# Kernel optimization log

Measured on AMD Instinct MI355X. Metric: run time of the kernel, lower is better.

## Reference

```python
import jax, jax.numpy as jnp
import numpy as np

V, D, B, P = 50000, 128, 1024, 50
N, E = B * P, B * P
SCALE = 12.0


def _norm(x):
    return jnp.linalg.norm(x, axis=-1, keepdims=True)


def setup_inputs():
    key = jax.random.key(0)
    ks = jax.random.split(key, 32)
    stdv = 1.0 / np.sqrt(D)

    def u(k, shape):
        return jax.random.uniform(k, shape, minval=-stdv, maxval=stdv, dtype=jnp.float32)

    iid = jax.random.randint(ks[0], (N,), 0, V)
    # edges stay inside each session's node block [g*P, (g+1)*P)
    base = jnp.repeat(jnp.arange(B) * P, P)
    edge_src = base + jax.random.randint(ks[1], (E,), 0, P)
    edge_dst = base + jax.random.randint(ks[2], (E,), 0, P)
    node_gid = jnp.repeat(jnp.arange(B), P)          # session id per node
    last_nodes = jnp.arange(B) * P + (P - 1)          # nodes with data['last']==1
    edge_w = jax.random.uniform(ks[3], (E,), minval=0.1, maxval=1.0)
    edge_t = jax.random.uniform(ks[4], (E,))
    params = dict(
        embedding=u(ks[5], (V, D)),
        W1=u(ks[6], (D, 2 * D)), W2=u(ks[7], (D, 2 * D)),
        gru_wih=u(ks[8], (3 * D, 4 * D)), gru_whh=u(ks[9], (3 * D, D)),
        gru_bih=u(ks[10], (3 * D,)), gru_bhh=u(ks[11], (3 * D,)),
        Wxr=u(ks[12], (D, D)), bxr=u(ks[13], (D,)),
        Wxz=u(ks[14], (D, D)), bxz=u(ks[15], (D,)),
        Wxh=u(ks[16], (D, D)), bxh=u(ks[17], (D,)),
        Whr=u(ks[18], (D, D)), bhr=u(ks[19], (D,)),
        Whz=u(ks[20], (D, D)), bhz=u(ks[21], (D,)),
        Whh=u(ks[22], (D, D)), bhh=u(ks[23], (D,)),
        fc_u=u(ks[24], (D, D)),
        fc_vw=u(ks[25], (D, D)), fc_vb=u(ks[26], (D,)),
        fc_e=u(ks[27], (D,)),
        fc_sr=u(ks[28], (2 * D, D)),
    )
    return dict(iid=iid, edge_src=edge_src, edge_dst=edge_dst, node_gid=node_gid,
                last_nodes=last_nodes, edge_w=edge_w, edge_t=edge_t, **params)


def reference(iid, edge_src, edge_dst, node_gid, last_nodes, edge_w, edge_t,
              embedding, W1, W2, gru_wih, gru_whh, gru_bih, gru_bhh,
              Wxr, bxr, Wxz, bxz, Wxh, bxh, Whr, bhr, Whz, bhz, Whh, bhh,
              fc_u, fc_vw, fc_vb, fc_e, fc_sr):
    segN = lambda d, ids: jax.ops.segment_sum(d, ids, num_segments=N)
    feat = embedding[iid]
    feat = feat / (_norm(feat) + 1e-12)

    # --- GGNNLayer (num_layers=1): weighted-mean over in-edges and reversed graph ---
    ws_in = segN(edge_w, edge_dst)
    ws_out = segN(edge_w, edge_src)
    m_in = segN(feat[edge_src] * edge_w[:, None], edge_dst)
    m_out = segN(feat[edge_dst] * edge_w[:, None], edge_src)
    neigh1 = m_in / jnp.where(ws_in > 0, ws_in, 1.0)[:, None]   # zero-degree -> 0 (DGL default)
    neigh2 = m_out / jnp.where(ws_out > 0, ws_out, 1.0)[:, None]
    hn = jnp.concatenate([neigh1 @ W1, neigh2 @ W2], axis=1)    # [N, 4D]
    gi = hn @ gru_wih.T + gru_bih
    gh = feat @ gru_whh.T + gru_bhh
    ir, iz, inn = jnp.split(gi, 3, axis=1)
    hr, hz, hnn = jnp.split(gh, 3, axis=1)
    r = jax.nn.sigmoid(ir + hr)
    z = jax.nn.sigmoid(iz + hz)
    n = jnp.tanh(inn + r * hnn)
    feat = (1.0 - z) * n + z * feat                              # GRUCell update
    feat = feat / jnp.maximum(_norm(feat), 1e-12)                # F.normalize

    # --- GraphGRUODE: one RK4 step on [0, t_end]; per-eval time-filtered symmetric GCN ---
    x = feat
    no_self = edge_src != edge_dst

    def gcn(h, em, W, b):
        # DGL GraphConv norm='both' on the masked graph + its reverse edges
        deg = segN(em, edge_src) + segN(em, edge_dst)
        nrm = jnp.maximum(deg, 1.0) ** -0.5
        hs = h * nrm[:, None]
        me = em[:, None]
        agg = segN(hs[edge_src] * me, edge_dst) + segN(hs[edge_dst] * me, edge_src)
        return (agg * nrm[:, None]) @ W + b

    def f(tv, h):
        em = ((edge_t <= tv) & no_self).astype(h.dtype)
        xr = gcn(x, em, Wxr, bxr)
        xz = gcn(x, em, Wxz, bxz)
        xh = gcn(x, em, Wxh, bxh)
        r_ = jax.nn.sigmoid(xr + gcn(h, em, Whr, bhr))
        z_ = jax.nn.sigmoid(xz + gcn(h, em, Whz, bhz))
        u_ = jnp.tanh(xh + gcn(r_ * h, em, Whh, bhh))
        dh = (1.0 - z_) * (u_ - h)
        return dh / jnp.maximum(_norm(dh), 1e-12)                # F.normalize

    dt = edge_t.max()
    k1 = f(jnp.float32(0.0), feat)
    k2 = f(dt * 0.5, feat + dt * 0.5 * k1)
    k3 = f(dt * 0.5, feat + dt * 0.5 * k2)
    k4 = f(dt, feat + dt * k3)
    feat = feat + (dt / 6.0) * (k1 + 2.0 * k2 + 2.0 * k3 + k4)
    feat = feat / _norm(feat)                                    # torch code divides with no eps here

    # --- AttnReadout (batch_norm disabled, fc_out is None) ---
    fu = feat @ fc_u
    fv = feat[last_nodes] @ fc_vw + fc_vb                        # [B, D]
    e = jax.nn.sigmoid(fu + fv[node_gid]) @ fc_e                 # [N]
    emax = jax.ops.segment_max(e, node_gid, num_segments=B)
    ee = jnp.exp(e - emax[node_gid])
    alpha = ee / jax.ops.segment_sum(ee, node_gid, num_segments=B)[node_gid]
    sr_g = jax.ops.segment_sum(feat * alpha[:, None], node_gid, num_segments=B)
    sr = jnp.concatenate([feat[last_nodes], sr_g], axis=1) @ fc_sr
    sr = sr / (_norm(sr) + 1e-12)

    target = embedding / (_norm(embedding) + 1e-12)
    logits = sr @ target.T                                       # [B, V]
    return jax.nn.log_softmax(SCALE * logits, axis=-1)
```

## Files before the change

kernel.cpp:

```cpp
#include <hip/hip_runtime.h>
#include <math.h>

constexpr int V_ = 50000, D_ = 128, B_ = 1024, P_ = 50;
constexpr int N_ = 51200, E_ = 51200;
constexpr long long NS_ = (long long)N_ * D_;
constexpr float SCALE_ = 12.0f;
constexpr int NBN_L = (V_ + 127) / 128;
constexpr int NBN_P = 392;

typedef unsigned short u16;
typedef __attribute__((ext_vector_type(8))) unsigned short u16x8;
typedef __attribute__((ext_vector_type(8))) __bf16 bf16x8;
typedef __attribute__((ext_vector_type(4))) float f32x4;

static __device__ __forceinline__ float wsum(float v) {
    #pragma unroll
    for (int o = 32; o; o >>= 1) v += __shfl_xor(v, o, 64);
    return v;
}
static __device__ __forceinline__ float wmax(float v) {
    #pragma unroll
    for (int o = 32; o; o >>= 1) v = fmaxf(v, __shfl_xor(v, o, 64));
    return v;
}
static __device__ __forceinline__ float fsig(float x) { return 1.f / (1.f + __expf(-x)); }
static __device__ __forceinline__ float ftanh(float x) { return 2.f / (1.f + __expf(-2.f * x)) - 1.f; }
static __device__ __forceinline__ u16 f2b(float x) {
    unsigned u = __float_as_uint(x);
    u += 0x7fffu + ((u >> 16) & 1u);
    return (u16)(u >> 16);
}
static __device__ __forceinline__ float b2f(u16 u) {
    return __uint_as_float(((unsigned)u) << 16);
}
static __device__ __forceinline__ float redlr(float v) {
    v += __shfl_xor(v, 1, 64); v += __shfl_xor(v, 2, 64);
    v += __shfl_xor(v, 4, 64); v += __shfl_xor(v, 8, 64);
    return v;
}

__global__ void k_embcv(const float* __restrict__ emb, u16* __restrict__ embb,
                        float* __restrict__ rnv) {
    int row = blockIdx.x * 4 + (threadIdx.x >> 6);
    if (row >= V_) return;
    int l = threadIdx.x & 63;
    const float* p = emb + (long long)row * D_;
    float a = p[l], b = p[l + 64];
    float ss = wsum(a * a + b * b);
    if (l == 0) rnv[row] = 1.f / (sqrtf(ss) + 1e-12f);
    u16* q = embb + (long long)row * D_;
    q[l] = f2b(a); q[l + 64] = f2b(b);
}

__global__ void k_dtmax(const float* __restrict__ et, float* __restrict__ dt) {
    __shared__ float s[1024];
    float m = 0.f;
    for (int i = threadIdx.x; i < E_; i += 1024) m = fmaxf(m, et[i]);
    s[threadIdx.x] = m; __syncthreads();
    for (int o = 512; o; o >>= 1) {
        if (threadIdx.x < o) s[threadIdx.x] = fmaxf(s[threadIdx.x], s[threadIdx.x + o]);
        __syncthreads();
    }
    if (threadIdx.x == 0) *dt = s[0];
}

__global__ void k_csr(const int* __restrict__ esrc, const int* __restrict__ edst,
                      const float* __restrict__ et, const float* __restrict__ dtp,
                      float* __restrict__ csr_nrm, int* __restrict__ csr_soff,
                      int* __restrict__ csr_snbr) {
    __shared__ int ses[P_], sed[P_], sdeg[P_], soff[P_ + 1];
    int mg = blockIdx.x, t = threadIdx.x;
    int mask = mg >> 10;
    int g = mg & 1023;
    int n0 = g * P_;
    float tfac = (mask == 0) ? 0.f : ((mask == 1) ? 0.5f : 1.f);
    float tv = tfac * dtp[0];
    if (t < P_) {
        int E0 = g * P_ + t;
        int s = esrc[E0] - n0, d = edst[E0] - n0;
        bool ml = (s != d) && (et[E0] <= tv);
        ses[t] = ml ? s : -1;
        sed[t] = ml ? d : -1;
    }
    __syncthreads();
    if (t < P_) {
        int dg = 0;
        for (int e = 0; e < P_; e++) dg += (ses[e] == t) + (sed[e] == t);
        sdeg[t] = dg;
        csr_nrm[(long long)mg * P_ + t] = rsqrtf(fmaxf((float)dg, 1.f));
    }
    __syncthreads();
    {
        int v = (t < P_) ? sdeg[t] : 0;
        int inc = v;
        #pragma unroll
        for (int o = 1; o < 64; o <<= 1) {
            int u = __shfl_up(inc, o, 64);
            if (t >= o) inc += u;
        }
        if (t < P_) soff[t] = inc - v;
        if (t == P_ - 1) soff[P_] = inc;
    }
    __syncthreads();
    if (t <= P_) csr_soff[(long long)mg * 64 + t] = soff[t];
    if (t < P_) {
        int c = soff[t];
        for (int e = 0; e < P_; e++) {
            if (ses[e] == t) csr_snbr[(long long)mg * 100 + (c++)] = sed[e];
            if (sed[e] == t) csr_snbr[(long long)mg * 100 + (c++)] = ses[e];
        }
    }
}

__global__ void k_feat0(const u16* __restrict__ embb, const float* __restrict__ rnv,
                        const int* __restrict__ iid, u16* __restrict__ featb) {
    int row = blockIdx.x * 4 + (threadIdx.x >> 6);
    int l = threadIdx.x & 63;
    int id = iid[row];
    const u16* p = embb + (long long)id * D_;
    float s = rnv[id];
    u16* qb = featb + (long long)row * D_;
    qb[l] = f2b(b2f(p[l]) * s); qb[l + 64] = f2b(b2f(p[l + 64]) * s);
}

__global__ void k_aggA_g(const int* __restrict__ esrc, const int* __restrict__ edst,
                         const float* __restrict__ ew, const u16* __restrict__ featb,
                         u16* __restrict__ m_in, u16* __restrict__ m_out) {
    __shared__ float sfeat[P_ * D_];
    __shared__ float smin[P_ * D_];
    __shared__ float smout[P_ * D_];
    __shared__ int ses[P_], sed[P_];
    __shared__ float sw[P_], swin[P_], swout[P_];
    int g = blockIdx.x, t = threadIdx.x;
    int n0 = g * P_;
    long long base = (long long)n0 * D_;
    for (int i = t; i < P_ * D_; i += 256) {
        sfeat[i] = b2f(featb[base + i]);
        smin[i] = 0.f; smout[i] = 0.f;
    }
    if (t < P_) {
        int E0 = g * P_ + t;
        ses[t] = esrc[E0] - n0;
        sed[t] = edst[E0] - n0;
        sw[t] = ew[E0];
    }
    __syncthreads();
    int d = t & 127;
    for (int e = 0; e < P_; e++) {
        int ls = ses[e], ld = sed[e];
        float w = sw[e];
        if (t < 128) smin[ld * D_ + d] += sfeat[ls * D_ + d] * w;
        else         smout[ls * D_ + d] += sfeat[ld * D_ + d] * w;
    }
    if (t < P_) {
        float wi = 0.f, wo = 0.f;
        for (int e = 0; e < P_; e++) {
            if (sed[e] == t) wi += sw[e];
            if (ses[e] == t) wo += sw[e];
        }
        swin[t] = (wi > 0.f) ? 1.f / wi : 1.f;
        swout[t] = (wo > 0.f) ? 1.f / wo : 1.f;
    }
    __syncthreads();
    for (int i = t; i < P_ * D_; i += 256) {
        int n = i >> 7;
        m_in[base + i] = f2b(smin[i] * swin[n]);
        m_out[base + i] = f2b(smout[i] * swout[n]);
    }
}

__global__ void k_prec_all(const float* __restrict__ W1, const float* __restrict__ W2,
                           const float* __restrict__ wih, const float* __restrict__ whh,
                           const float* __restrict__ bih, const float* __restrict__ bhh,
                           const float* __restrict__ Wxr, const float* __restrict__ Wxz,
                           const float* __restrict__ Whr, const float* __restrict__ Whz,
                           const float* __restrict__ bxr, const float* __restrict__ bxz,
                           const float* __restrict__ bhr, const float* __restrict__ bhz,
                           const float* __restrict__ Wxh, const float* __restrict__ Whh,
                           const float* __restrict__ bxh, const float* __restrict__ bhh2,
                           const float* __restrict__ fcu,
                           u16* __restrict__ BM1t, u16* __restrict__ BM2t, u16* __restrict__ BM3t,
                           u16* __restrict__ Brz1, u16* __restrict__ Brz2,
                           u16* __restrict__ Bu1, u16* __restrict__ Bu2, u16* __restrict__ Bfc,
                           float* __restrict__ b512, float* __restrict__ brz,
                           float* __restrict__ bu) {
    int blk = blockIdx.x, t = threadIdx.x;
    if (blk < 512) {
        const float* W = (blk < 256) ? W1 : W2;
        int coff = (blk < 256) ? 0 : 256;
        u16* Bt = (blk < 256) ? BM1t : BM2t;
        int idx = (blk & 255) * 256 + t;
        int j = idx >> 7, k = idx & 127;
        float s = 0.f;
        if (j < 384) {
            const float* wr = W + (long long)k * 256;
            const float* ir = wih + (long long)j * 512 + coff;
            for (int c = 0; c < 256; c++) s += wr[c] * ir[c];
        }
        Bt[idx] = f2b(s);
    } else if (blk < 768) {
        int idx = (blk - 512) * 256 + t;
        int j = idx >> 7, k = idx & 127;
        float v = 0.f;
        if (j < 256) v = whh[(long long)j * 128 + k];
        else if (j >= 384) v = whh[(long long)(j - 128) * 128 + k];
        BM3t[idx] = f2b(v);
    } else if (blk < 896) {
        int idx = (blk - 768) * 256 + t;
        int c = idx >> 7, k = idx & 127;
        float v1 = (c < 128) ? Wxr[(long long)k * 128 + c] : Wxz[(long long)k * 128 + (c - 128)];
        float v2 = (c < 128) ? Whr[(long long)k * 128 + c] : Whz[(long long)k * 128 + (c - 128)];
        Brz1[idx] = f2b(v1); Brz2[idx] = f2b(v2);
        if (k == 0) brz[c] = (c < 128) ? bxr[c] + bhr[c] : bxz[c - 128] + bhz[c - 128];
    } else if (blk < 960) {
        int idx = (blk - 896) * 256 + t;
        int c = idx >> 7, k = idx & 127;
        Bu1[idx] = f2b(Wxh[(long long)k * 128 + c]);
        Bu2[idx] = f2b(Whh[(long long)k * 128 + c]);
        if (k == 0) bu[c] = bxh[c] + bhh2[c];
    } else if (blk < 1024) {
        int idx = (blk - 960) * 256 + t;
        int c = idx >> 7, k = idx & 127;
        Bfc[idx] = f2b(fcu[(long long)k * 128 + c]);
    } else {
        int j = (blk - 1024) * 256 + t;
        if (j < 512) {
            float v;
            if (j < 256) v = bih[j] + bhh[j];
            else if (j < 384) v = bih[j];
            else v = bhh[j - 128];
            b512[j] = v;
        }
    }
}

template<int NSEG, int ACT>
__launch_bounds__(256)
__global__ void k_mm(const u16* __restrict__ A1, const u16* __restrict__ A2,
                     const u16* __restrict__ A3,
                     const u16* __restrict__ B1, const u16* __restrict__ B2,
                     const u16* __restrict__ B3,
                     const float* __restrict__ bias,
                     u16* __restrict__ C, int ldc, int nbn) {
    __shared__ u16 As[128 * 40];
    __shared__ u16 Bs[128 * 40];
    const int t = threadIdx.x;
    const int bid = blockIdx.x;
    const int xcd = bid & 7, idx = bid >> 3;
    const int nbm8 = gridDim.x / (8 * nbn);
    const int bm = xcd * nbm8 + idx / nbn;
    const int bn = idx % nbn;
    const int lane = t & 63, wid = t >> 6;
    const int wr = wid >> 1, wc = wid & 1;
    const int lr = lane & 15, lh = lane >> 4;
    f32x4 acc[4][4] = {};
    constexpr int KTOT = NSEG * 128;
    for (int ks = 0; ks < KTOT; ks += 32) {
        const u16* Ap = (NSEG == 1) ? A1 : (ks < 128 ? A1 : (ks < 256 ? A2 : A3));
        const u16* Bp = (NSEG == 1) ? B1 : (ks < 128 ? B1 : (ks < 256 ? B2 : B3));
        int kk = ks & 127;
        #pragma unroll
        for (int i = 0; i < 2; i++) {
            int id2 = i * 256 + t;
            int row = id2 >> 2, kl = (id2 & 3) * 8;
            u16x8 va = *(const u16x8*)&Ap[((long long)bm * 128 + row) * 128 + kk + kl];
            *(u16x8*)&As[row * 40 + kl] = va;
            u16x8 vb = *(const u16x8*)&Bp[((long long)bn * 128 + row) * 128 + kk + kl];
            *(u16x8*)&Bs[row * 40 + kl] = vb;
        }
        __syncthreads();
        bf16x8 af[4], bf[4];
        #pragma unroll
        for (int f = 0; f < 4; f++) {
            u16x8 ar = *(const u16x8*)&As[(wr * 64 + f * 16 + lr) * 40 + lh * 8];
            u16x8 br = *(const u16x8*)&Bs[(wc * 64 + f * 16 + lr) * 40 + lh * 8];
            af[f] = __builtin_bit_cast(bf16x8, ar);
            bf[f] = __builtin_bit_cast(bf16x8, br);
        }
        #pragma unroll
        for (int fr = 0; fr < 4; fr++)
            #pragma unroll
            for (int fc = 0; fc < 4; fc++)
                acc[fr][fc] = __builtin_amdgcn_mfma_f32_16x16x32_bf16(af[fr], bf[fc], acc[fr][fc], 0, 0, 0);
        __syncthreads();
    }
    #pragma unroll
    for (int fc = 0; fc < 4; fc++) {
        int col = bn * 128 + wc * 64 + fc * 16 + lr;
        float bb = bias ? bias[col] : 0.f;
        #pragma unroll
        for (int fr = 0; fr < 4; fr++) {
            int rowl = wr * 64 + fr * 16 + lh * 4;
            long long row0 = (long long)bm * 128 + rowl;
            #pragma unroll
            for (int r = 0; r < 4; r++) {
                float v = acc[fr][fc][r] + bb;
                if (ACT == 1) v = fsig(v);
                else if (ACT == 2) v = ftanh(v);
                C[(row0 + r) * (long long)ldc + col] = f2b(v);
            }
        }
    }
}

__global__ void k_gru2(const u16* __restrict__ gih, u16* __restrict__ featb,
                       u16* __restrict__ hb) {
    int row = blockIdx.x * 4 + (threadIdx.x >> 6);
    int l = threadIdx.x & 63;
    const u16* g = gih + (long long)row * 512;
    u16* fb = featb + (long long)row * 128;
    float nv[2]; float ss = 0.f;
    #pragma unroll
    for (int tq = 0; tq < 2; tq++) {
        int d = l + tq * 64;
        float r = fsig(b2f(g[d]));
        float z = fsig(b2f(g[128 + d]));
        float n = ftanh(b2f(g[256 + d]) + r * b2f(g[384 + d]));
        float fv = b2f(fb[d]);
        nv[tq] = (1.f - z) * n + z * fv;
        ss += nv[tq] * nv[tq];
    }
    ss = wsum(ss);
    float s = 1.f / fmaxf(sqrtf(ss), 1e-12f);
    u16 a = f2b(nv[0] * s), b = f2b(nv[1] * s);
    fb[l] = a; fb[l + 64] = b;
    u16* hh = hb + (long long)row * 128;
    hh[l] = a; hh[l + 64] = b;
}

template<int FIN>
__launch_bounds__(512, 8)
__global__ void k_fstep(const float* __restrict__ csr_nrm, const int* __restrict__ csr_soff,
                        const int* __restrict__ csr_snbr, int mask,
                        const float* __restrict__ dtp,
                        int h_is_x, int axmode,
                        u16* __restrict__ featb, u16* __restrict__ hb,
                        u16* __restrict__ AXg, u16* __restrict__ RHG, u16* __restrict__ ZG,
                        u16* __restrict__ accg,
                        const u16* __restrict__ Brz1, const u16* __restrict__ Brz2,
                        const float* __restrict__ brz,
                        const u16* __restrict__ Bu1, const u16* __restrict__ Bu2,
                        const float* __restrict__ bu,
                        float accw, float hfac, int first) {
    constexpr int AS = 136;
    __shared__ u16 sAX[64 * AS];
    __shared__ u16 sAH[64 * AS];
    __shared__ float snrm[P_];
    __shared__ int soff[P_ + 1], snbr[2 * P_];
    __shared__ float ssqW[4][64];
    const int g = blockIdx.x, t = threadIdx.x;
    const int n0 = g * P_;
    const long long base = (long long)n0 * D_;
    const int wv = t >> 6, lane = t & 63;
    const int lr = lane & 15, lh = lane >> 4;
    const float dt = dtp[0];
    const long long mg = (long long)(mask * 1024 + g);

    for (int i = t; i < 64 * AS; i += 512) { sAX[i] = 0; sAH[i] = 0; }
    if (t < P_) snrm[t] = csr_nrm[mg * P_ + t];
    if (t <= P_) soff[t] = csr_soff[mg * 64 + t];
    if (t >= 64 && t < 64 + 2 * P_) snbr[t - 64] = csr_snbr[mg * 100 + (t - 64)];
    __syncthreads();

    const int d = t & 127, grp = t >> 7;
    const int nlo = grp * 13, nhi = (grp * 13 + 13 < P_) ? grp * 13 + 13 : P_;
    if (axmode == 2) {
        for (int n = nlo; n < nhi; n++)
            sAX[n * AS + d] = AXg[base + (long long)n * D_ + d];
    } else {
        for (int n = nlo; n < nhi; n++) {
            float a = 0.f;
            for (int j = soff[n]; j < soff[n + 1]; j++) {
                int nb = snbr[j];
                a += b2f(featb[base + (long long)nb * D_ + d]) * snrm[nb];
            }
            u16 v = f2b(a * snrm[n]);
            sAX[n * AS + d] = v;
            if (axmode == 1) AXg[base + (long long)n * D_ + d] = v;
        }
    }
    if (!h_is_x) {
        for (int n = nlo; n < nhi; n++) {
            float a = 0.f;
            for (int j = soff[n]; j < soff[n + 1]; j++) {
                int nb = snbr[j];
                a += b2f(hb[base + (long long)nb * D_ + d]) * snrm[nb];
            }
            sAH[n * AS + d] = f2b(a * snrm[n]);
        }
    }
    __syncthreads();
    {
        const u16* A2 = h_is_x ? sAX : sAH;
        f32x4 acc[4][2] = {};
        for (int ks = 0; ks < 256; ks += 32) {
            const u16* Ap = (ks < 128) ? sAX : A2;
            const u16* Bp = (ks < 128) ? Brz1 : Brz2;
            int kk = ks & 127;
            bf16x8 af[4], bf[2];
            #pragma unroll
            for (int f = 0; f < 4; f++) {
                u16x8 ar = *(const u16x8*)&Ap[(f * 16 + lr) * AS + kk + lh * 8];
                af[f] = __builtin_bit_cast(bf16x8, ar);
            }
            #pragma unroll
            for (int f = 0; f < 2; f++) {
                int col = wv * 32 + f * 16 + lr;
                u16x8 br = *(const u16x8*)&Bp[(long long)col * 128 + kk + lh * 8];
                bf[f] = __builtin_bit_cast(bf16x8, br);
            }
            #pragma unroll
            for (int fr = 0; fr < 4; fr++)
                #pragma unroll
                for (int fc = 0; fc < 2; fc++)
                    acc[fr][fc] = __builtin_amdgcn_mfma_f32_16x16x32_bf16(af[fr], bf[fc], acc[fr][fc], 0, 0, 0);
        }
        #pragma unroll
        for (int fc = 0; fc < 2; fc++) {
            int col = wv * 32 + fc * 16 + lr;
            float bb = brz[col];
            #pragma unroll
            for (int fr = 0; fr < 4; fr++) {
                int row0 = fr * 16 + lh * 4;
                #pragma unroll
                for (int r = 0; r < 4; r++) {
                    int row = row0 + r;
                    if (row < P_) {
                        float v = fsig(acc[fr][fc][r] + bb);
                        long long ix = base + (long long)row * D_;
                        if (col < 128) RHG[ix + col] = f2b(v * b2f(hb[ix + col]));
                        else           ZG[ix + col - 128] = f2b(v);
                    }
                }
            }
        }
    }
    __syncthreads();
    for (int n = nlo; n < nhi; n++) {
        float a = 0.f;
        for (int j = soff[n]; j < soff[n + 1]; j++) {
            int nb = snbr[j];
            a += b2f(RHG[base + (long long)nb * D_ + d]) * snrm[nb];
        }
        sAH[n * AS + d] = f2b(a * snrm[n]);
    }
    __syncthreads();
    const int wr = wv >> 2, wc = wv & 3;
    f32x4 acc[2][2] = {};
    for (int ks = 0; ks < 256; ks += 32) {
        const u16* Ap = (ks < 128) ? sAX : sAH;
        const u16* Bp = (ks < 128) ? Bu1 : Bu2;
        int kk = ks & 127;
        bf16x8 af[2], bf[2];
        #pragma unroll
        for (int f = 0; f < 2; f++) {
            u16x8 ar = *(const u16x8*)&Ap[(wr * 32 + f * 16 + lr) * AS + kk + lh * 8];
            af[f] = __builtin_bit_cast(bf16x8, ar);
        }
        #pragma unroll
        for (int f = 0; f < 2; f++) {
            int col = wc * 32 + f * 16 + lr;
            u16x8 br = *(const u16x8*)&Bp[(long long)col * 128 + kk + lh * 8];
            bf[f] = __builtin_bit_cast(bf16x8, br);
        }
        #pragma unroll
        for (int fr = 0; fr < 2; fr++)
            #pragma unroll
            for (int fc = 0; fc < 2; fc++)
                acc[fr][fc] = __builtin_amdgcn_mfma_f32_16x16x32_bf16(af[fr], bf[fc], acc[fr][fc], 0, 0, 0);
    }
    float pr[2][4] = {};
    #pragma unroll
    for (int fc = 0; fc < 2; fc++) {
        int col = wc * 32 + fc * 16 + lr;
        float bb = bu[col];
        #pragma unroll
        for (int fr = 0; fr < 2; fr++) {
            int row0 = wr * 32 + fr * 16 + lh * 4;
            #pragma unroll
            for (int r = 0; r < 4; r++) {
                int row = row0 + r;
                float v = 0.f;
                if (row < P_) {
                    long long ix = base + (long long)row * D_ + col;
                    float u = ftanh(acc[fr][fc][r] + bb);
                    float z = b2f(ZG[ix]);
                    float hh = b2f(hb[ix]);
                    v = (1.f - z) * (u - hh);
                }
                acc[fr][fc][r] = v;
                pr[fr][r] += v * v;
            }
        }
    }
    #pragma unroll
    for (int fr = 0; fr < 2; fr++)
        #pragma unroll
        for (int r = 0; r < 4; r++) {
            float v = redlr(pr[fr][r]);
            if (lr == 0) ssqW[wc][wr * 32 + fr * 16 + lh * 4 + r] = v;
        }
    __syncthreads();
    if (FIN) {
        float dt6 = dt / 6.f;
        float pr2[2][4] = {};
        #pragma unroll
        for (int fr = 0; fr < 2; fr++) {
            int row0 = wr * 32 + fr * 16 + lh * 4;
            #pragma unroll
            for (int r = 0; r < 4; r++) {
                int row = row0 + r;
                float sc = 0.f;
                if (row < P_) {
                    float ssum = ssqW[0][row] + ssqW[1][row] + ssqW[2][row] + ssqW[3][row];
                    sc = 1.f / fmaxf(sqrtf(ssum), 1e-12f);
                }
                #pragma unroll
                for (int fc = 0; fc < 2; fc++) {
                    int col = wc * 32 + fc * 16 + lr;
                    float fv2 = 0.f;
                    if (row < P_) {
                        long long ix = base + (long long)row * D_ + col;
                        float kv = acc[fr][fc][r] * sc;
                        float an = b2f(accg[ix]) + accw * kv;
                        fv2 = b2f(featb[ix]) + dt6 * an;
                    }
                    acc[fr][fc][r] = fv2;
                    pr2[fr][r] += fv2 * fv2;
                }
            }
        }
        __syncthreads();
        #pragma unroll
        for (int fr = 0; fr < 2; fr++)
            #pragma unroll
            for (int r = 0; r < 4; r++) {
                float v = redlr(pr2[fr][r]);
                if (lr == 0) ssqW[wc][wr * 32 + fr * 16 + lh * 4 + r] = v;
            }
        __syncthreads();
        #pragma unroll
        for (int fr = 0; fr < 2; fr++) {
            int row0 = wr * 32 + fr * 16 + lh * 4;
            #pragma unroll
            for (int r = 0; r < 4; r++) {
                int row = row0 + r;
                if (row >= P_) continue;
                float ssum = ssqW[0][row] + ssqW[1][row] + ssqW[2][row] + ssqW[3][row];
                float s2 = 1.f / sqrtf(ssum);
                #pragma unroll
                for (int fc = 0; fc < 2; fc++) {
                    int col = wc * 32 + fc * 16 + lr;
                    featb[base + (long long)row * D_ + col] = f2b(acc[fr][fc][r] * s2);
                }
            }
        }
    } else {
        #pragma unroll
        for (int fr = 0; fr < 2; fr++) {
            int row0 = wr * 32 + fr * 16 + lh * 4;
            #pragma unroll
            for (int r = 0; r < 4; r++) {
                int row = row0 + r;
                if (row >= P_) continue;
                float ssum = ssqW[0][row] + ssqW[1][row] + ssqW[2][row] + ssqW[3][row];
                float sc = 1.f / fmaxf(sqrtf(ssum), 1e-12f);
                #pragma unroll
                for (int fc = 0; fc < 2; fc++) {
                    int col = wc * 32 + fc * 16 + lr;
                    long long ix = base + (long long)row * D_ + col;
                    float kv = acc[fr][fc][r] * sc;
                    float an = (first ? 0.f : b2f(accg[ix])) + accw * kv;
                    accg[ix] = f2b(an);
                    hb[ix] = f2b(b2f(featb[ix]) + hfac * dt * kv);
                }
            }
        }
    }
}

__launch_bounds__(256)
__global__ void k_readout(const u16* __restrict__ featb, const u16* __restrict__ FU,
                          const int* __restrict__ last,
                          const float* __restrict__ fvw, const float* __restrict__ fvbv,
                          const float* __restrict__ fce, const float* __restrict__ fsr,
                          u16* __restrict__ srb) {
    __shared__ float sfl[128], sfv[128], se[64], sal[64], sin2[256], red[2];
    int g = blockIdx.x, t = threadIdx.x;
    int n0 = g * P_;
    long long ln = last[g];
    if (t < 128) sfl[t] = b2f(featb[ln * 128 + t]);
    __syncthreads();
    if (t < 128) {
        float s = fvbv[t];
        for (int k = 0; k < 128; k++) s += sfl[k] * fvw[(long long)k * 128 + t];
        sfv[t] = s;
        sin2[t] = sfl[t];
    }
    __syncthreads();
    int wid = t >> 6, lane = t & 63;
    float fce0 = fce[lane], fce1 = fce[lane + 64];
    for (int p = wid; p < P_; p += 4) {
        const u16* fu = FU + (long long)(n0 + p) * 128;
        float x0 = b2f(fu[lane]) + sfv[lane];
        float x1 = b2f(fu[lane + 64]) + sfv[lane + 64];
        float s = fsig(x0) * fce0 + fsig(x1) * fce1;
        s = wsum(s);
        if (lane == 0) se[p] = s;
    }
    __syncthreads();
    if (t < 64) {
        float v = (t < P_) ? se[t] : -1e30f;
        float m = wmax(v);
        float ex = (t < P_) ? __expf(v - m) : 0.f;
        float ss = wsum(ex);
        if (t < P_) sal[t] = ex / ss;
    }
    __syncthreads();
    if (t < 128) {
        float s = 0.f;
        for (int p = 0; p < P_; p++)
            s += b2f(featb[(long long)(n0 + p) * 128 + t]) * sal[p];
        sin2[128 + t] = s;
    }
    __syncthreads();
    if (t < 128) {
        float s = 0.f;
        for (int k = 0; k < 256; k++) s += sin2[k] * fsr[(long long)k * 128 + t];
        float ss = wsum(s * s);
        if (lane == 0) red[t >> 6] = ss;
        __syncthreads();
        float nrm = sqrtf(red[0] + red[1]);
        srb[(long long)g * 128 + t] = f2b(s / (nrm + 1e-12f));
    } else {
        __syncthreads();
    }
}

template<int PASS>
__launch_bounds__(256)
__global__ void k_logits(const u16* __restrict__ A, const u16* __restrict__ Bt,
                         const float* __restrict__ rnv, float* __restrict__ rowsumP,
                         const float* __restrict__ logz, float* __restrict__ C) {
    __shared__ u16 As[128 * 40];
    __shared__ u16 Bs[128 * 40];
    __shared__ float sredW[2][128];
    const int t = threadIdx.x;
    const int bid = blockIdx.x;
    const int xcd = bid & 7, idx = bid >> 3;
    const int bm = idx & 7, bnl = idx >> 3;
    const int bn = xcd * 49 + bnl;
    if (bn >= NBN_L) return;
    const int lane = t & 63, wid = t >> 6;
    const int wr = wid >> 1, wc = wid & 1;
    const int lr = lane & 15, lh = lane >> 4;
    f32x4 acc[4][4] = {};
    for (int ks = 0; ks < 128; ks += 32) {
        #pragma unroll
        for (int i = 0; i < 2; i++) {
            int id2 = i * 256 + t;
            int row = id2 >> 2, kl = (id2 & 3) * 8;
            u16x8 va = *(const u16x8*)&A[((long long)bm * 128 + row) * 128 + ks + kl];
            *(u16x8*)&As[row * 40 + kl] = va;
            long long gcol = (long long)bn * 128 + row;
            u16x8 vb;
            if (gcol < V_) vb = *(const u16x8*)&Bt[gcol * 128 + ks + kl];
            else vb = u16x8{0, 0, 0, 0, 0, 0, 0, 0};
            *(u16x8*)&Bs[row * 40 + kl] = vb;
        }
        __syncthreads();
        bf16x8 af[4], bf[4];
        #pragma unroll
        for (int f = 0; f < 4; f++) {
            u16x8 ar = *(const u16x8*)&As[(wr * 64 + f * 16 + lr) * 40 + lh * 8];
            u16x8 br = *(const u16x8*)&Bs[(wc * 64 + f * 16 + lr) * 40 + lh * 8];
            af[f] = __builtin_bit_cast(bf16x8, ar);
            bf[f] = __builtin_bit_cast(bf16x8, br);
        }
        #pragma unroll
        for (int fr = 0; fr < 4; fr++)
            #pragma unroll
            for (int fc = 0; fc < 4; fc++)
                acc[fr][fc] = __builtin_amdgcn_mfma_f32_16x16x32_bf16(af[fr], bf[fc], acc[fr][fc], 0, 0, 0);
        __syncthreads();
    }
    if (PASS == 0) {
        float pr[4][4] = {};
        #pragma unroll
        for (int fc = 0; fc < 4; fc++) {
            int col = bn * 128 + wc * 64 + fc * 16 + lr;
            if (col >= V_) continue;
            float cs = rnv[col] * SCALE_;
            #pragma unroll
            for (int fr = 0; fr < 4; fr++)
                #pragma unroll
                for (int r = 0; r < 4; r++)
                    pr[fr][r] += __expf(acc[fr][fc][r] * cs - SCALE_);
        }
        #pragma unroll
        for (int fr = 0; fr < 4; fr++)
            #pragma unroll
            for (int r = 0; r < 4; r++) {
                float v = redlr(pr[fr][r]);
                if (lr == 0) sredW[wc][wr * 64 + fr * 16 + lh * 4 + r] = v;
            }
        __syncthreads();
        if (t < 128) rowsumP[(long long)(bm * 128 + t) * NBN_P + bn] = sredW[0][t] + sredW[1][t];
    } else {
        if (t < 128) sredW[0][t] = logz[bm * 128 + t];
        __syncthreads();
        #pragma unroll
        for (int fc = 0; fc < 4; fc++) {
            int col = bn * 128 + wc * 64 + fc * 16 + lr;
            if (col >= V_) continue;
            float cs = rnv[col] * SCALE_;
            #pragma unroll
            for (int fr = 0; fr < 4; fr++) {
                int rowl = wr * 64 + fr * 16 + lh * 4;
                long long row0 = (long long)bm * 128 + rowl;
                #pragma unroll
                for (int r = 0; r < 4; r++)
                    C[(row0 + r) * (long long)V_ + col] = acc[fr][fc][r] * cs - SCALE_ - sredW[0][rowl + r];
            }
        }
    }
}

__global__ void k_rsum(const float* __restrict__ rowsumP, float* __restrict__ logz) {
    int t = threadIdx.x;
    int row = blockIdx.x * 128 + (t >> 1);
    int half = t & 1;
    const float* p = rowsumP + (long long)row * NBN_P;
    float s = 0.f;
    int j0 = half ? 196 : 0, j1 = half ? NBN_L : 196;
    for (int j = j0; j < j1; j++) s += p[j];
    s += __shfl_xor(s, 1);
    if (!half) logz[row] = logf(s);
}

extern "C" void kernel_launch(void* const* d_in, const int* in_sizes, int n_in,
                              void* d_out, int out_size, void* d_ws, size_t ws_size,
                              hipStream_t stream) {
    const int* iid   = (const int*)d_in[0];
    const int* esrc  = (const int*)d_in[1];
    const int* edst  = (const int*)d_in[2];
    const int* last  = (const int*)d_in[4];
    const float* ew  = (const float*)d_in[5];
    const float* et  = (const float*)d_in[6];
    const float* emb = (const float*)d_in[7];
    const float* W1  = (const float*)d_in[8];
    const float* W2  = (const float*)d_in[9];
    const float* wih = (const float*)d_in[10];
    const float* whh = (const float*)d_in[11];
    const float* bih = (const float*)d_in[12];
    const float* bhh = (const float*)d_in[13];
    const float* Wxr = (const float*)d_in[14]; const float* bxr = (const float*)d_in[15];
    const float* Wxz = (const float*)d_in[16]; const float* bxz = (const float*)d_in[17];
    const float* Wxh = (const float*)d_in[18]; const float* bxh = (const float*)d_in[19];
    const float* Whr = (const float*)d_in[20]; const float* bhr = (const float*)d_in[21];
    const float* Whz = (const float*)d_in[22]; const float* bhz = (const float*)d_in[23];
    const float* Whh = (const float*)d_in[24]; const float* bhh2 = (const float*)d_in[25];
    const float* fcu = (const float*)d_in[26];
    const float* fvw = (const float*)d_in[27]; const float* fvbv = (const float*)d_in[28];
    const float* fce = (const float*)d_in[29];
    const float* fsr = (const float*)d_in[30];
    float* out = (float*)d_out;

    char* w = (char*)d_ws;
    auto alloc = [&](size_t bytes) { char* p = w; w += (bytes + 255) & ~(size_t)255; return p; };
    u16* ACCb    = (u16*)alloc(NS_ * 2);
    u16* FEATb   = (u16*)alloc(NS_ * 2);
    u16* Hb      = (u16*)alloc(NS_ * 2);
    u16* MINb    = (u16*)alloc(NS_ * 2);
    u16* MOUTb   = (u16*)alloc(NS_ * 2);
    u16* GIHb    = (u16*)alloc(NS_ * 8);
    u16* AXb     = GIHb;
    u16* RHG     = GIHb + NS_;
    u16* ZG      = GIHb + 2 * NS_;
    u16* FUb     = MINb;
    u16* embb    = (u16*)alloc((long long)V_ * 128 * 2);
    u16* srb     = (u16*)alloc(B_ * 128 * 2);
    u16* BM1t    = (u16*)alloc(512 * 128 * 2);
    u16* BM2t    = (u16*)alloc(512 * 128 * 2);
    u16* BM3t    = (u16*)alloc(512 * 128 * 2);
    u16* Brz1    = (u16*)alloc(256 * 128 * 2);
    u16* Brz2    = (u16*)alloc(256 * 128 * 2);
    u16* Bu1     = (u16*)alloc(128 * 128 * 2);
    u16* Bu2     = (u16*)alloc(128 * 128 * 2);
    u16* Bfc     = (u16*)alloc(128 * 128 * 2);
    float* b512  = (float*)alloc(512 * 4);
    float* brz   = (float*)alloc(256 * 4);
    float* bu    = (float*)alloc(128 * 4);
    float* dtp   = (float*)alloc(64 * 4);
    float* rnv   = (float*)alloc((long long)V_ * 4);
    float* rowsumP = (float*)alloc((long long)B_ * NBN_P * 4);
    float* logz  = (float*)alloc(B_ * 4);
    float* csr_nrm = (float*)alloc(3LL * B_ * P_ * 4);
    int* csr_soff  = (int*)alloc(3LL * B_ * 64 * 4);
    int* csr_snbr  = (int*)alloc(3LL * B_ * 100 * 4);

    k_embcv<<<(V_ + 3) / 4, 256, 0, stream>>>(emb, embb, rnv);
    k_dtmax<<<1, 1024, 0, stream>>>(et, dtp);
    k_csr<<<3 * B_, 64, 0, stream>>>(esrc, edst, et, dtp, csr_nrm, csr_soff, csr_snbr);
    k_feat0<<<N_ / 4, 256, 0, stream>>>(embb, rnv, iid, FEATb);

    k_aggA_g<<<B_, 256, 0, stream>>>(esrc, edst, ew, FEATb, MINb, MOUTb);
    k_prec_all<<<1026, 256, 0, stream>>>(W1, W2, wih, whh, bih, bhh,
                                         Wxr, Wxz, Whr, Whz, bxr, bxz, bhr, bhz,
                                         Wxh, Whh, bxh, bhh2, fcu,
                                         BM1t, BM2t, BM3t, Brz1, Brz2, Bu1, Bu2, Bfc,
                                         b512, brz, bu);
    k_mm<3, 0><<<1600, 256, 0, stream>>>(MINb, MOUTb, FEATb, BM1t, BM2t, BM3t, b512, GIHb, 512, 4);
    k_gru2<<<N_ / 4, 256, 0, stream>>>(GIHb, FEATb, Hb);

    k_fstep<0><<<B_, 512, 0, stream>>>(csr_nrm, csr_soff, csr_snbr, 0, dtp, 1, 0,
                                       FEATb, Hb, AXb, RHG, ZG, ACCb,
                                       Brz1, Brz2, brz, Bu1, Bu2, bu, 1.f, 0.5f, 1);
    k_fstep<0><<<B_, 512, 0, stream>>>(csr_nrm, csr_soff, csr_snbr, 1, dtp, 0, 1,
                                       FEATb, Hb, AXb, RHG, ZG, ACCb,
                                       Brz1, Brz2, brz, Bu1, Bu2, bu, 2.f, 0.5f, 0);
    k_fstep<0><<<B_, 512, 0, stream>>>(csr_nrm, csr_soff, csr_snbr, 1, dtp, 0, 2,
                                       FEATb, Hb, AXb, RHG, ZG, ACCb,
                                       Brz1, Brz2, brz, Bu1, Bu2, bu, 2.f, 1.0f, 0);
    k_fstep<1><<<B_, 512, 0, stream>>>(csr_nrm, csr_soff, csr_snbr, 2, dtp, 0, 0,
                                       FEATb, Hb, AXb, RHG, ZG, ACCb,
                                       Brz1, Brz2, brz, Bu1, Bu2, bu, 1.f, 0.0f, 0);

    k_mm<1, 0><<<400, 256, 0, stream>>>(FEATb, nullptr, nullptr, Bfc, nullptr, nullptr,
                                        nullptr, FUb, 128, 1);
    k_readout<<<B_, 256, 0, stream>>>(FEATb, FUb, last, fvw, fvbv, fce, fsr, srb);

    k_logits<0><<<3136, 256, 0, stream>>>(srb, embb, rnv, rowsumP, nullptr, nullptr);
    k_rsum<<<8, 256, 0, stream>>>(rowsumP, logz);
    k_logits<1><<<3136, 256, 0, stream>>>(srb, embb, rnv, nullptr, logz, out);
}
```

Baseline: 664.7 us.

## Stage session tiles in shared memory and keep r*h gating on-chip in fstep

Each k_fstep block now loads its session's feature or hidden tile into a new shared buffer sT, so the neighbour gathers read shared memory instead of scattered global loads. The r*h product is written back into sT rather than a global RHG buffer, which removes a global write/read round trip and the RHG allocation. The extra ~13.6KB of shared memory per block may lower occupancy, and the added barriers serialize the load and gather phases.

```diff
diff --git a/kernel.cpp b/kernel.cpp
--- a/kernel.cpp
+++ b/kernel.cpp
@@ -335,7 +335,7 @@
                         const float* __restrict__ dtp,
                         int h_is_x, int axmode,
                         u16* __restrict__ featb, u16* __restrict__ hb,
-                        u16* __restrict__ AXg, u16* __restrict__ RHG, u16* __restrict__ ZG,
+                        u16* __restrict__ AXg, u16* __restrict__ ZG,
                         u16* __restrict__ accg,
                         const u16* __restrict__ Brz1, const u16* __restrict__ Brz2,
                         const float* __restrict__ brz,
@@ -345,6 +345,7 @@
     constexpr int AS = 136;
     __shared__ u16 sAX[64 * AS];
     __shared__ u16 sAH[64 * AS];
+    __shared__ u16 sT[P_ * AS];
     __shared__ float snrm[P_];
     __shared__ int soff[P_ + 1], snbr[2 * P_];
     __shared__ float ssqW[4][64];
@@ -360,34 +361,54 @@
     if (t < P_) snrm[t] = csr_nrm[mg * P_ + t];
     if (t <= P_) soff[t] = csr_soff[mg * 64 + t];
     if (t >= 64 && t < 64 + 2 * P_) snbr[t - 64] = csr_snbr[mg * 100 + (t - 64)];
-    __syncthreads();
 
     const int d = t & 127, grp = t >> 7;
     const int nlo = grp * 13, nhi = (grp * 13 + 13 < P_) ? grp * 13 + 13 : P_;
+
+#define LOAD_TILE(SRC)                                                           \
+    for (int i = t; i < P_ * D_; i += 512)                                       \
+        sT[(i >> 7) * AS + (i & 127)] = (SRC)[base + i];
+
+#define GATHER_TO(DST)                                                           \
+    for (int n = nlo; n < nhi; n++) {                                            \
+        float a = 0.f;                                                           \
+        for (int j = soff[n]; j < soff[n + 1]; j++) {                            \
+            int nb = snbr[j];                                                    \
+            a += b2f(sT[nb * AS + d]) * snrm[nb];                                \
+        }                                                                        \
+        DST[n * AS + d] = f2b(a * snrm[n]);                                      \
+    }
+
     if (axmode == 2) {
         for (int n = nlo; n < nhi; n++)
             sAX[n * AS + d] = AXg[base + (long long)n * D_ + d];
     } else {
-        for (int n = nlo; n < nhi; n++) {
-            float a = 0.f;
-            for (int j = soff[n]; j < soff[n + 1]; j++) {
-                int nb = snbr[j];
-                a += b2f(featb[base + (long long)nb * D_ + d]) * snrm[nb];
-            }
-            u16 v = f2b(a * snrm[n]);
-            sAX[n * AS + d] = v;
-            if (axmode == 1) AXg[base + (long long)n * D_ + d] = v;
-        }
+        LOAD_TILE(featb)
+        __syncthreads();
+        if (axmode == 1) {
+            for (int n = nlo; n < nhi; n++) {
+                float a = 0.f;
+                for (int j = soff[n]; j < soff[n + 1]; j++) {
+                    int nb = snbr[j];
+                    a += b2f(sT[nb * AS + d]) * snrm[nb];
+                }
+                u16 v = f2b(a * snrm[n]);
+                sAX[n * AS + d] = v;
+                AXg[base + (long long)n * D_ + d] = v;
+            }
+        } else {
+            GATHER_TO(sAX)
+        }
+        __syncthreads();
     }
     if (!h_is_x) {
-        for (int n = nlo; n < nhi; n++) {
-            float a = 0.f;
-            for (int j = soff[n]; j < soff[n + 1]; j++) {
-                int nb = snbr[j];
-                a += b2f(hb[base + (long long)nb * D_ + d]) * snrm[nb];
-            }
-            sAH[n * AS + d] = f2b(a * snrm[n]);
-        }
+        LOAD_TILE(hb)
+    } else if (axmode == 2) {
+        LOAD_TILE(featb)
+    }
+    __syncthreads();
+    if (!h_is_x) {
+        GATHER_TO(sAH)
     }
     __syncthreads();
     {
@@ -427,23 +448,21 @@
                     int row = row0 + r;
                     if (row < P_) {
                         float v = fsig(acc[fr][fc][r] + bb);
-                        long long ix = base + (long long)row * D_;
-                        if (col < 128) RHG[ix + col] = f2b(v * b2f(hb[ix + col]));
-                        else           ZG[ix + col - 128] = f2b(v);
+                        if (col < 128) {
+                            int sx = row * AS + col;
+                            sT[sx] = f2b(v * b2f(sT[sx]));
+                        } else {
+                            ZG[base + (long long)row * D_ + col - 128] = f2b(v);
+                        }
                     }
                 }
             }
         }
     }
     __syncthreads();
-    for (int n = nlo; n < nhi; n++) {
-        float a = 0.f;
-        for (int j = soff[n]; j < soff[n + 1]; j++) {
-            int nb = snbr[j];
-            a += b2f(RHG[base + (long long)nb * D_ + d]) * snrm[nb];
-        }
-        sAH[n * AS + d] = f2b(a * snrm[n]);
-    }
+    GATHER_TO(sAH)
+#undef GATHER_TO
+#undef LOAD_TILE
     __syncthreads();
     const int wr = wv >> 2, wc = wv & 3;
     f32x4 acc[2][2] = {};
@@ -485,7 +504,7 @@
                     long long ix = base + (long long)row * D_ + col;
                     float u = ftanh(acc[fr][fc][r] + bb);
                     float z = b2f(ZG[ix]);
-                    float hh = b2f(hb[ix]);
+                    float hh = h_is_x ? b2f(featb[ix]) : b2f(hb[ix]);
                     v = (1.f - z) * (u - hh);
                 }
                 acc[fr][fc][r] = v;
@@ -775,8 +794,7 @@
     u16* MOUTb   = (u16*)alloc(NS_ * 2);
     u16* GIHb    = (u16*)alloc(NS_ * 8);
     u16* AXb     = GIHb;
-    u16* RHG     = GIHb + NS_;
-    u16* ZG      = GIHb + 2 * NS_;
+    u16* ZG      = GIHb + NS_;
     u16* FUb     = MINb;
     u16* embb    = (u16*)alloc((long long)V_ * 128 * 2);
     u16* srb     = (u16*)alloc(B_ * 128 * 2);
@@ -814,16 +832,16 @@
     k_gru2<<<N_ / 4, 256, 0, stream>>>(GIHb, FEATb, Hb);
 
     k_fstep<0><<<B_, 512, 0, stream>>>(csr_nrm, csr_soff, csr_snbr, 0, dtp, 1, 0,
-                                       FEATb, Hb, AXb, RHG, ZG, ACCb,
+                                       FEATb, Hb, AXb, ZG, ACCb,
                                        Brz1, Brz2, brz, Bu1, Bu2, bu, 1.f, 0.5f, 1);
     k_fstep<0><<<B_, 512, 0, stream>>>(csr_nrm, csr_soff, csr_snbr, 1, dtp, 0, 1,
-                                       FEATb, Hb, AXb, RHG, ZG, ACCb,
+                                       FEATb, Hb, AXb, ZG, ACCb,
                                        Brz1, Brz2, brz, Bu1, Bu2, bu, 2.f, 0.5f, 0);
     k_fstep<0><<<B_, 512, 0, stream>>>(csr_nrm, csr_soff, csr_snbr, 1, dtp, 0, 2,
-                                       FEATb, Hb, AXb, RHG, ZG, ACCb,
+                                       FEATb, Hb, AXb, ZG, ACCb,
                                        Brz1, Brz2, brz, Bu1, Bu2, bu, 2.f, 1.0f, 0);
     k_fstep<1><<<B_, 512, 0, stream>>>(csr_nrm, csr_soff, csr_snbr, 2, dtp, 0, 0,
-                                       FEATb, Hb, AXb, RHG, ZG, ACCb,
+                                       FEATb, Hb, AXb, ZG, ACCb,
                                        Brz1, Brz2, brz, Bu1, Bu2, bu, 1.f, 0.0f, 0);
 
     k_mm<1, 0><<<400, 256, 0, stream>>>(FEATb, nullptr, nullptr, Bfc, nullptr, nullptr,
```

After: 689.9 us. +3.8%, slower.
